# Performance work log

Measured on AMD Instinct MI355X. Metric: run time of the kernel, lower is better.

## Reference

```python
import jax, jax.numpy as jnp
import numpy as np

N_NODES = 100000
D_FEAT = 128
N_EDGES = 800000


def setup_inputs() -> dict:
    key = jax.random.key(0)
    k_h, k_src, k_dst, k_w = jax.random.split(key, 4)
    h = jax.random.normal(k_h, (N_NODES, D_FEAT), dtype=jnp.float32)
    src = jax.random.randint(k_src, (N_EDGES,), 0, N_NODES, dtype=jnp.int64)
    dst = jax.random.randint(k_dst, (N_EDGES,), 0, N_NODES, dtype=jnp.int64)
    # nn.Linear(2*D_FEAT, 1): weight [1, 2*D_FEAT], bias [1]
    bound = 1.0 / np.sqrt(2 * D_FEAT)
    W = jax.random.uniform(k_w, (1, 2 * D_FEAT), dtype=jnp.float32, minval=-bound, maxval=bound)
    b = jnp.zeros((1,), dtype=jnp.float32)
    return {"h": h, "src": src, "dst": dst, "W": W, "b": b}


def reference(h, src, dst, W, b):
    # Split W so we never materialize the [E, 2d] concat:
    # cat([h_u, h_v]) @ W.T == h_u @ W_u.T + h_v @ W_v.T
    W_u = W[:, :D_FEAT]   # [1, d]
    W_v = W[:, D_FEAT:]   # [1, d]
    # Per-edge gather + tiny matvec -> score [E, 1]
    score = h[src] @ W_u.T + h[dst] @ W_v.T + b
    # Global min-max normalization; min/max computed on detached score
    s = jax.lax.stop_gradient(score)
    s_min = jnp.min(s)
    s_max = jnp.max(s)
    score = (score - s_min) / (s_max - s_min)
    return score
```

## Files before the change

### kernel.cpp

```cpp
#include <hip/hip_runtime.h>

#define D_FEAT 128

__global__ __launch_bounds__(256) void proj_kernel(
    const float* __restrict__ h,
    const float* __restrict__ W,
    const float* __restrict__ bptr,
    float* __restrict__ pu,
    float* __restrict__ pv,
    int n_nodes)
{
    const int t    = threadIdx.x & 7;
    const int node = blockIdx.x * 32 + (threadIdx.x >> 3);
    if (node >= n_nodes) return;

    const float4* W4 = (const float4*)W;
    float4 wu[4], wv[4];
    #pragma unroll
    for (int j = 0; j < 4; ++j) {
        wu[j] = W4[j * 8 + t];
        wv[j] = W4[32 + j * 8 + t];
    }

    const float4* h4 = (const float4*)(h + (size_t)node * D_FEAT);
    float4 hv[4];
    #pragma unroll
    for (int j = 0; j < 4; ++j) hv[j] = h4[j * 8 + t];

    float su = 0.f, sv = 0.f;
    #pragma unroll
    for (int j = 0; j < 4; ++j) {
        su += hv[j].x*wu[j].x + hv[j].y*wu[j].y + hv[j].z*wu[j].z + hv[j].w*wu[j].w;
        sv += hv[j].x*wv[j].x + hv[j].y*wv[j].y + hv[j].z*wv[j].z + hv[j].w*wv[j].w;
    }
    #pragma unroll
    for (int off = 4; off > 0; off >>= 1) {
        su += __shfl_xor(su, off, 64);
        sv += __shfl_xor(sv, off, 64);
    }
    if (t == 0) {
        pu[node] = su + bptr[0];
        pv[node] = sv;
    }
}

__global__ __launch_bounds__(256) void score_kernel(
    const int*   __restrict__ src,
    const int*   __restrict__ dst,
    const float* __restrict__ pu,
    const float* __restrict__ pv,
    float*       __restrict__ out,
    float*       __restrict__ pmin,
    float*       __restrict__ pmax,
    int n_edges)
{
    const int i = blockIdx.x * blockDim.x + threadIdx.x;
    float vmin =  3.4028235e38f;
    float vmax = -3.4028235e38f;
    if (i < n_edges) {
        const float s = pu[src[i]] + pv[dst[i]];
        out[i] = s;
        vmin = s;
        vmax = s;
    }
    #pragma unroll
    for (int off = 32; off > 0; off >>= 1) {
        vmin = fminf(vmin, __shfl_xor(vmin, off, 64));
        vmax = fmaxf(vmax, __shfl_xor(vmax, off, 64));
    }
    __shared__ float smin[4], smax[4];
    const int w = threadIdx.x >> 6;
    if ((threadIdx.x & 63) == 0) { smin[w] = vmin; smax[w] = vmax; }
    __syncthreads();
    if (threadIdx.x == 0) {
        pmin[blockIdx.x] = fminf(fminf(smin[0], smin[1]), fminf(smin[2], smin[3]));
        pmax[blockIdx.x] = fmaxf(fmaxf(smax[0], smax[1]), fmaxf(smax[2], smax[3]));
    }
}

__global__ __launch_bounds__(256) void norm_kernel(
    float* __restrict__ out,
    const float* __restrict__ pmin,
    const float* __restrict__ pmax,
    int nblk, int n4, int n_edges)
{
    float vmin =  3.4028235e38f;
    float vmax = -3.4028235e38f;
    for (int i = threadIdx.x; i < nblk; i += 256) {
        vmin = fminf(vmin, pmin[i]);
        vmax = fmaxf(vmax, pmax[i]);
    }
    #pragma unroll
    for (int off = 32; off > 0; off >>= 1) {
        vmin = fminf(vmin, __shfl_xor(vmin, off, 64));
        vmax = fmaxf(vmax, __shfl_xor(vmax, off, 64));
    }
    __shared__ float smin[4], smax[4];
    const int w = threadIdx.x >> 6;
    if ((threadIdx.x & 63) == 0) { smin[w] = vmin; smax[w] = vmax; }
    __syncthreads();
    const float mn  = fminf(fminf(smin[0], smin[1]), fminf(smin[2], smin[3]));
    const float mx  = fmaxf(fmaxf(smax[0], smax[1]), fmaxf(smax[2], smax[3]));
    const float inv = 1.0f / (mx - mn);

    const int i = blockIdx.x * blockDim.x + threadIdx.x;
    if (i >= n4) return;
    float4 v = ((const float4*)out)[i];
    v.x = (v.x - mn) * inv;
    v.y = (v.y - mn) * inv;
    v.z = (v.z - mn) * inv;
    v.w = (v.w - mn) * inv;
    ((float4*)out)[i] = v;
    if (i == n4 - 1) {
        for (int e = n4 * 4; e < n_edges; ++e)
            out[e] = (out[e] - mn) * inv;
    }
}

extern "C" void kernel_launch(void* const* d_in, const int* in_sizes, int n_in,
                              void* d_out, int out_size, void* d_ws, size_t ws_size,
                              hipStream_t stream) {
    const float* h   = (const float*)d_in[0];
    const int*   src = (const int*)d_in[1];
    const int*   dst = (const int*)d_in[2];
    const float* W   = (const float*)d_in[3];
    const float* b   = (const float*)d_in[4];
    float* out = (float*)d_out;

    const int n_nodes = in_sizes[0] / D_FEAT;
    const int n_edges = in_sizes[1];

    const int blk2 = (n_edges + 255) / 256;

    float* ws   = (float*)d_ws;
    float* pu   = ws;
    float* pv   = ws + n_nodes;
    float* pmin = ws + 2 * n_nodes;
    float* pmax = pmin + blk2;

    {
        const int blocks = (n_nodes + 31) / 32;
        proj_kernel<<<blocks, 256, 0, stream>>>(h, W, b, pu, pv, n_nodes);
    }
    score_kernel<<<blk2, 256, 0, stream>>>(src, dst, pu, pv, out, pmin, pmax, n_edges);
    {
        const int n4 = n_edges >> 2;
        const int blocks = (n4 + 255) / 256;
        norm_kernel<<<blocks, 256, 0, stream>>>(out, pmin, pmax, blk2, n4, n_edges);
    }
}
```

Baseline: 30.13 us.

## Fuse score and normalization into one persistent kernel with grid-wide sync

Replaces the score and norm kernels with a single kernel of 256 persistent blocks. Each thread keeps 13 edge scores in registers, and per-block min/max partials are combined through an atomic counter. The last block to arrive reduces the partials and publishes min and inverse range, while the other blocks spin-wait before writing normalized outputs. This removes one launch and the write-then-reread of the intermediate scores. The cost is a software grid barrier that depends on all 256 blocks being resident at once, and a hardcoded edges-per-thread limit of 256*256*13 edges.

```diff
diff --git a/kernel.cpp b/kernel.cpp
--- a/kernel.cpp
+++ b/kernel.cpp
@@ -1,6 +1,8 @@
 #include <hip/hip_runtime.h>
 
-#define D_FEAT 128
+#define D_FEAT  128
+#define NBLK    256
+#define EPT     13
 
 __global__ __launch_bounds__(256) void proj_kernel(
     const float* __restrict__ h,
@@ -8,8 +10,11 @@
     const float* __restrict__ bptr,
     float* __restrict__ pu,
     float* __restrict__ pv,
+    unsigned* __restrict__ syncc,
     int n_nodes)
 {
+    if (blockIdx.x == 0 && threadIdx.x == 0) { syncc[0] = 0u; syncc[1] = 0u; }
+
     const int t    = threadIdx.x & 7;
     const int node = blockIdx.x * 32 + (threadIdx.x >> 3);
     if (node >= n_nodes) return;
@@ -44,24 +49,33 @@
     }
 }
 
-__global__ __launch_bounds__(256) void score_kernel(
+__global__ __launch_bounds__(256) void fused_score_norm_kernel(
     const int*   __restrict__ src,
     const int*   __restrict__ dst,
     const float* __restrict__ pu,
     const float* __restrict__ pv,
     float*       __restrict__ out,
-    float*       __restrict__ pmin,
-    float*       __restrict__ pmax,
+    unsigned long long* __restrict__ partials,
+    unsigned long long* __restrict__ gcell,
+    unsigned* __restrict__ syncc,
     int n_edges)
 {
-    const int i = blockIdx.x * blockDim.x + threadIdx.x;
+    const int tid    = blockIdx.x * 256 + threadIdx.x;
+    const int stride = NBLK * 256;
+
+    float sc[EPT];
     float vmin =  3.4028235e38f;
     float vmax = -3.4028235e38f;
-    if (i < n_edges) {
-        const float s = pu[src[i]] + pv[dst[i]];
-        out[i] = s;
-        vmin = s;
-        vmax = s;
+    #pragma unroll
+    for (int k = 0; k < EPT; ++k) {
+        const int e = tid + k * stride;
+        float s = 0.f;
+        if (e < n_edges) {
+            s = pu[src[e]] + pv[dst[e]];
+            vmin = fminf(vmin, s);
+            vmax = fmaxf(vmax, s);
+        }
+        sc[k] = s;
     }
     #pragma unroll
     for (int off = 32; off > 0; off >>= 1) {
@@ -69,51 +83,73 @@
         vmax = fmaxf(vmax, __shfl_xor(vmax, off, 64));
     }
     __shared__ float smin[4], smax[4];
+    __shared__ int   isred;
+    __shared__ unsigned g_lo, g_hi;
     const int w = threadIdx.x >> 6;
     if ((threadIdx.x & 63) == 0) { smin[w] = vmin; smax[w] = vmax; }
     __syncthreads();
+
     if (threadIdx.x == 0) {
-        pmin[blockIdx.x] = fminf(fminf(smin[0], smin[1]), fminf(smin[2], smin[3]));
-        pmax[blockIdx.x] = fmaxf(fmaxf(smax[0], smax[1]), fmaxf(smax[2], smax[3]));
+        const float a = fminf(fminf(smin[0], smin[1]), fminf(smin[2], smin[3]));
+        const float m = fmaxf(fmaxf(smax[0], smax[1]), fmaxf(smax[2], smax[3]));
+        const unsigned long long p =
+            ((unsigned long long)__float_as_uint(m) << 32) | __float_as_uint(a);
+        __hip_atomic_exchange(&partials[blockIdx.x], p,
+                              __ATOMIC_RELEASE, __HIP_MEMORY_SCOPE_AGENT);
+        const unsigned old = __hip_atomic_fetch_add(&syncc[0], 1u,
+                              __ATOMIC_ACQ_REL, __HIP_MEMORY_SCOPE_AGENT);
+        isred = (old == NBLK - 1);
     }
-}
+    __syncthreads();
 
-__global__ __launch_bounds__(256) void norm_kernel(
-    float* __restrict__ out,
-    const float* __restrict__ pmin,
-    const float* __restrict__ pmax,
-    int nblk, int n4, int n_edges)
-{
-    float vmin =  3.4028235e38f;
-    float vmax = -3.4028235e38f;
-    for (int i = threadIdx.x; i < nblk; i += 256) {
-        vmin = fminf(vmin, pmin[i]);
-        vmax = fmaxf(vmax, pmax[i]);
+    if (isred) {
+        const unsigned long long p = __hip_atomic_load(&partials[threadIdx.x],
+                              __ATOMIC_ACQUIRE, __HIP_MEMORY_SCOPE_AGENT);
+        float a = __uint_as_float((unsigned)(p & 0xFFFFFFFFull));
+        float m = __uint_as_float((unsigned)(p >> 32));
+        #pragma unroll
+        for (int off = 32; off > 0; off >>= 1) {
+            a = fminf(a, __shfl_xor(a, off, 64));
+            m = fmaxf(m, __shfl_xor(m, off, 64));
+        }
+        if ((threadIdx.x & 63) == 0) { smin[w] = a; smax[w] = m; }
+        __syncthreads();
+        if (threadIdx.x == 0) {
+            const float mn  = fminf(fminf(smin[0], smin[1]), fminf(smin[2], smin[3]));
+            const float mx  = fmaxf(fmaxf(smax[0], smax[1]), fmaxf(smax[2], smax[3]));
+            const float inv = 1.0f / (mx - mn);
+            const unsigned long long gv =
+                ((unsigned long long)__float_as_uint(inv) << 32) | __float_as_uint(mn);
+            __hip_atomic_exchange(gcell, gv,
+                                  __ATOMIC_RELEASE, __HIP_MEMORY_SCOPE_AGENT);
+            __hip_atomic_store(&syncc[1], 1u,
+                               __ATOMIC_RELEASE, __HIP_MEMORY_SCOPE_AGENT);
+        }
+        __syncthreads();
+    } else {
+        if (threadIdx.x == 0) {
+            while (__hip_atomic_load(&syncc[1], __ATOMIC_RELAXED,
+                                     __HIP_MEMORY_SCOPE_AGENT) == 0u)
+                __builtin_amdgcn_s_sleep(2);
+            (void)__hip_atomic_load(&syncc[1], __ATOMIC_ACQUIRE,
+                                    __HIP_MEMORY_SCOPE_AGENT);
+        }
+        __syncthreads();
     }
+
+    if (threadIdx.x == 0) {
+        const unsigned long long gv = __hip_atomic_load(gcell,
+                              __ATOMIC_ACQUIRE, __HIP_MEMORY_SCOPE_AGENT);
+        g_lo = (unsigned)(gv & 0xFFFFFFFFull);
+        g_hi = (unsigned)(gv >> 32);
+    }
+    __syncthreads();
+    const float mn  = __uint_as_float(g_lo);
+    const float inv = __uint_as_float(g_hi);
     #pragma unroll
-    for (int off = 32; off > 0; off >>= 1) {
-        vmin = fminf(vmin, __shfl_xor(vmin, off, 64));
-        vmax = fmaxf(vmax, __shfl_xor(vmax, off, 64));
-    }
-    __shared__ float smin[4], smax[4];
-    const int w = threadIdx.x >> 6;
-    if ((threadIdx.x & 63) == 0) { smin[w] = vmin; smax[w] = vmax; }
-    __syncthreads();
-    const float mn  = fminf(fminf(smin[0], smin[1]), fminf(smin[2], smin[3]));
-    const float mx  = fmaxf(fmaxf(smax[0], smax[1]), fmaxf(smax[2], smax[3]));
-    const float inv = 1.0f / (mx - mn);
-
-    const int i = blockIdx.x * blockDim.x + threadIdx.x;
-    if (i >= n4) return;
-    float4 v = ((const float4*)out)[i];
-    v.x = (v.x - mn) * inv;
-    v.y = (v.y - mn) * inv;
-    v.z = (v.z - mn) * inv;
-    v.w = (v.w - mn) * inv;
-    ((float4*)out)[i] = v;
-    if (i == n4 - 1) {
-        for (int e = n4 * 4; e < n_edges; ++e)
-            out[e] = (out[e] - mn) * inv;
+    for (int k = 0; k < EPT; ++k) {
+        const int e = tid + k * stride;
+        if (e < n_edges) out[e] = (sc[k] - mn) * inv;
     }
 }
 
@@ -130,22 +166,17 @@
     const int n_nodes = in_sizes[0] / D_FEAT;
     const int n_edges = in_sizes[1];
 
-    const int blk2 = (n_edges + 255) / 256;
-
-    float* ws   = (float*)d_ws;
-    float* pu   = ws;
-    float* pv   = ws + n_nodes;
-    float* pmin = ws + 2 * n_nodes;
-    float* pmax = pmin + blk2;
+    float* ws = (float*)d_ws;
+    float* pu = ws;
+    float* pv = ws + n_nodes;
+    unsigned long long* partials = (unsigned long long*)(ws + 2 * n_nodes);
+    unsigned long long* gcell    = partials + NBLK;
+    unsigned*           syncc    = (unsigned*)(gcell + 1);
 
     {
         const int blocks = (n_nodes + 31) / 32;
-        proj_kernel<<<blocks, 256, 0, stream>>>(h, W, b, pu, pv, n_nodes);
+        proj_kernel<<<blocks, 256, 0, stream>>>(h, W, b, pu, pv, syncc, n_nodes);
     }
-    score_kernel<<<blk2, 256, 0, stream>>>(src, dst, pu, pv, out, pmin, pmax, n_edges);
-    {
-        const int n4 = n_edges >> 2;
-        const int blocks = (n4 + 255) / 256;
-        norm_kernel<<<blocks, 256, 0, stream>>>(out, pmin, pmax, blk2, n4, n_edges);
-    }
+    fused_score_norm_kernel<<<NBLK, 256, 0, stream>>>(
+        src, dst, pu, pv, out, partials, gcell, syncc, n_edges);
 }
```

Measured after the change: 48.63 us. 1.61x slower.
